# Kernel optimization log

Hardware: AMD Instinct MI355X
Metric: run time of the kernel (lower is better)

## Reference

```python
import jax, jax.numpy as jnp
import numpy as np
import itertools

B, RES, RES_, STRIDE = 256, 14, 7, 2
N, N_ = RES * RES, RES_ * RES_
IN_DIM, OUT_DIM = 384, 512
H, KD, AR = 12, 32, 2
D = AR * KD            # 64, per-head value dim
DH = D * H             # 768
NH_KD = KD * H         # 384
KV_H = DH + NH_KD      # 1152
EPS = 1e-5


def _bias_idxs():
    # Replicates the relative-offset indexing from __init__.
    points = list(itertools.product(range(RES), range(RES)))
    points_ = list(itertools.product(range(RES_), range(RES_)))
    offsets, idxs = {}, []
    for p1 in points_:
        for p2 in points:
            off = (abs(p1[0] * STRIDE - p2[0]), abs(p1[1] * STRIDE - p2[1]))
            if off not in offsets:
                offsets[off] = len(offsets)
            idxs.append(offsets[off])
    return np.array(idxs, dtype=np.int32).reshape(N_, N), len(offsets)


def linear_bn(x, w, gamma, beta, mean, var):
    # Linear (no bias) followed by BatchNorm1d in inference form (fused affine).
    s = gamma / jnp.sqrt(var + EPS)
    return jnp.matmul(x, w.T) * s + (beta - mean * s)


def setup_inputs() -> dict:
    key = jax.random.key(0)
    ks = jax.random.split(key, 12)
    idxs_np, n_off = _bias_idxs()

    def bn_params(k, dim):
        k1, k2, k3, k4 = jax.random.split(k, 4)
        return (jax.random.normal(k1, (dim,)) * 0.1 + 1.0,   # gamma
                jax.random.normal(k2, (dim,)) * 0.1,          # beta
                jax.random.normal(k3, (dim,)) * 0.1,          # running_mean
                jax.random.uniform(k4, (dim,), minval=0.5, maxval=1.5))  # running_var

    kv_g, kv_b, kv_m, kv_v = bn_params(ks[1], KV_H)
    q_g, q_b, q_m, q_v = bn_params(ks[3], NH_KD)
    pr_g, pr_b, pr_m, pr_v = bn_params(ks[5], OUT_DIM)

    return {
        "x": jax.random.normal(ks[0], (B, N, IN_DIM), dtype=jnp.float32),
        "kv_w": jax.random.normal(ks[6], (KV_H, IN_DIM), dtype=jnp.float32) * (IN_DIM ** -0.5),
        "kv_g": kv_g, "kv_b": kv_b, "kv_m": kv_m, "kv_v": kv_v,
        "q_w": jax.random.normal(ks[7], (NH_KD, IN_DIM), dtype=jnp.float32) * (IN_DIM ** -0.5),
        "q_g": q_g, "q_b": q_b, "q_m": q_m, "q_v": q_v,
        "proj_w": jax.random.normal(ks[8], (OUT_DIM, DH), dtype=jnp.float32) * (DH ** -0.5),
        "proj_g": pr_g, "proj_b": pr_b, "proj_m": pr_m, "proj_v": pr_v,
        "attention_biases": jax.random.normal(ks[9], (H, n_off), dtype=jnp.float32) * 0.02,
        "bias_idxs": jnp.asarray(idxs_np),
    }


def reference(x, kv_w, kv_g, kv_b, kv_m, kv_v,
              q_w, q_g, q_b, q_m, q_v,
              proj_w, proj_g, proj_b, proj_m, proj_v,
              attention_biases, bias_idxs):
    Bsz = x.shape[0]
    scale = KD ** -0.5
    # kv projection: [B, N, H, KD+D] -> split into k, v
    kv = linear_bn(x, kv_w, kv_g, kv_b, kv_m, kv_v).reshape(Bsz, N, H, KD + D)
    k, v = kv[..., :KD], kv[..., KD:]
    # strided subsample of queries: [B, 14, 14, C] -> [B, 49, C]
    xs = x.reshape(Bsz, RES, RES, IN_DIM)[:, ::STRIDE, ::STRIDE].reshape(Bsz, N_, IN_DIM)
    q = linear_bn(xs, q_w, q_g, q_b, q_m, q_v).reshape(Bsz, N_, H, KD)
    # attention with gathered relative-position bias: bias [H, N_, N]
    bias = attention_biases[:, bias_idxs]
    attn = jnp.einsum('bqhd,bkhd->bhqk', q, k) * scale + bias
    attn = jax.nn.softmax(attn, axis=-1)
    out = jnp.einsum('bhqk,bkhd->bqhd', attn, v).reshape(Bsz, N_, DH)
    out = jax.nn.hard_swish(out)
    return linear_bn(out, proj_w, proj_g, proj_b, proj_m, proj_v)
```

## Files before the change

kernel.cpp:

```cpp
#include <hip/hip_runtime.h>
#include <hip/hip_bf16.h>
#include <math.h>

typedef unsigned short U16;
typedef unsigned int U32;
typedef __attribute__((ext_vector_type(8))) short bf8;
typedef __attribute__((ext_vector_type(4))) float f4;
typedef __attribute__((ext_vector_type(4))) unsigned short u16x4;

#define AS1 __attribute__((address_space(1)))
#define AS3 __attribute__((address_space(3)))

#define BSZ   256
#define NTOK  196
#define NQ    49
#define INDIM 384
#define OUTD  512
#define NH    12
#define DV    64
#define DHD   768
#define KVH   1152
#define NPADR 224

__device__ inline U16 f2bf(float f){
    __hip_bfloat16 h = __float2bfloat16(f);
    return *(U16*)&h;
}
__device__ inline f4 f4zero(){ f4 z; z[0]=0.f; z[1]=0.f; z[2]=0.f; z[3]=0.f; return z; }
__device__ inline bf8 bf8zero(){ bf8 v;
#pragma unroll
    for (int j=0;j<8;++j) v[j]=0; return v; }

__global__ void k_cast8p(const float* __restrict__ in, U16* __restrict__ out, int n8){
    int i = blockIdx.x*256 + threadIdx.x;
    if (i >= n8) return;
    int rall = i / 48;
    int c8   = i - rall*48;
    int b    = rall / NPADR;
    int r    = rall - b*NPADR;
    U16 o[8];
    if (r < NTOK){
        const float* p = in + ((size_t)(b*NTOK + r))*INDIM + c8*8;
#pragma unroll
        for (int j=0;j<8;++j) o[j] = f2bf(p[j]);
    } else {
#pragma unroll
        for (int j=0;j<8;++j) o[j] = 0;
    }
    *(bf8*)(out + (size_t)i*8) = *(const bf8*)o;
}

#define W1C (KVH*INDIM/8)
#define W2C (INDIM*INDIM/8)
#define W3C (OUTD*DHD/8)
__global__ void k_castw(const float* __restrict__ w1, const float* __restrict__ w2,
                        const float* __restrict__ w3, U16* __restrict__ o1,
                        U16* __restrict__ o2, U16* __restrict__ o3){
    int i = blockIdx.x*256 + threadIdx.x;
    const float* p; U16* o;
    if (i < W1C){ p = w1 + (size_t)i*8; o = o1 + (size_t)i*8; }
    else if (i < W1C+W2C){ int k=i-W1C; p = w2 + (size_t)k*8; o = o2 + (size_t)k*8; }
    else if (i < W1C+W2C+W3C){ int k=i-W1C-W2C; p = w3 + (size_t)k*8; o = o3 + (size_t)k*8; }
    else return;
    U16 t[8];
#pragma unroll
    for (int j=0;j<8;++j) t[j] = f2bf(p[j]);
    *(bf8*)o = *(const bf8*)t;
}

#define BIAS_N   (NH*NQ*NTOK)
#define BIAS_BLK ((BIAS_N+255)/256)
#define BN_BLK   ((KVH+INDIM+OUTD)/256)
__global__ void k_misc(const float* __restrict__ ab, const int* __restrict__ idxs, int n_off,
                       const float* __restrict__ g1, const float* __restrict__ b1,
                       const float* __restrict__ m1, const float* __restrict__ v1,
                       const float* __restrict__ g2, const float* __restrict__ b2,
                       const float* __restrict__ m2, const float* __restrict__ v2,
                       const float* __restrict__ g3, const float* __restrict__ b3,
                       const float* __restrict__ m3, const float* __restrict__ v3,
                       float* __restrict__ s1, float* __restrict__ bo1,
                       float* __restrict__ s2, float* __restrict__ bo2,
                       float* __restrict__ s3, float* __restrict__ bo3,
                       float* __restrict__ bias_out){
    int blk = blockIdx.x;
    int tid = threadIdx.x;
    if (blk < BIAS_BLK){
        int i = blk*256 + tid;
        if (i < BIAS_N){
            int h = i / (NQ*NTOK);
            int qk = i - h*(NQ*NTOK);
            bias_out[i] = ab[h*n_off + idxs[qk]];
        }
    } else {
        int i = (blk-BIAS_BLK)*256 + tid;
        const float *g,*b,*m,*v; float *so,*bo; int k;
        if (i < KVH){ g=g1;b=b1;m=m1;v=v1;so=s1;bo=bo1;k=i; }
        else if (i < KVH+INDIM){ g=g2;b=b2;m=m2;v=v2;so=s2;bo=bo2;k=i-KVH; }
        else { g=g3;b=b3;m=m3;v=v3;so=s3;bo=bo3;k=i-KVH-INDIM; }
        float s = g[k] / sqrtf(v[k] + 1e-5f);
        so[k] = s;
        bo[k] = b[k] - m[k]*s;
    }
}

#define KLO 12800
__global__ __launch_bounds__(256,2) void k_fused(
    const U16* __restrict__ xbf, const U16* __restrict__ kvw, const U16* __restrict__ qo_,
    const float* __restrict__ skv, const float* __restrict__ bkv,
    const float* __restrict__ biasf, U16* __restrict__ aout)
{
    __shared__ U16 smem[20480];
    const int hw = blockIdx.x;
    const int bh = (hw & 7)*384 + (hw >> 3);
    const int b = bh / NH, h = bh - b*NH;
    const int tid = threadIdx.x, lane = tid & 63, w = tid >> 6;
    const int wm = w & 1, wn = w >> 1;
    const int l15 = lane & 15, oct = lane >> 4;

    U16* Ab[2] = { smem + 0,     smem + 7168 };
    U16* Bb[2] = { smem + 14336, smem + 17408 };

    U32 aoff[4];
#pragma unroll
    for (int c=0;c<3;++c){
        int s = c*256 + tid;
        int ach = s / NPADR, ar = s - ach*NPADR;
        aoff[c] = (U32)(b*NPADR + ar)*INDIM + ach*8;
    }
    {
        int s = 768 + (tid & 127);
        int ach = s / NPADR, ar = s - ach*NPADR;
        aoff[3] = (U32)(b*NPADR + ar)*INDIM + ach*8;
    }
    U32 boff[2];
    {
        int s0 = tid;
        int bc0 = s0 / 96, br0 = s0 - bc0*96;
        boff[0] = (U32)(h*96 + br0)*INDIM + bc0*8;
        int s1 = 128 + (tid | 128);
        int bc1 = s1 / 96, br1 = s1 - bc1*96;
        boff[1] = (U32)(h*96 + br1)*INDIM + bc1*8;
    }

    f4 acc[7][3];
#pragma unroll
    for (int i=0;i<7;++i)
#pragma unroll
        for (int j=0;j<3;++j) acc[i][j] = f4zero();

#define STAGE(buf, kb) do{ \
    _Pragma("unroll") \
    for (int c=0;c<3;++c) \
        __builtin_amdgcn_global_load_lds((const AS1 U32*)(xbf + aoff[c] + (kb)), \
            (AS3 U32*)(Ab[buf] + (c*256+tid)*8), 16, 0, 0); \
    if (tid < 128) \
        __builtin_amdgcn_global_load_lds((const AS1 U32*)(xbf + aoff[3] + (kb)), \
            (AS3 U32*)(Ab[buf] + (768+tid)*8), 16, 0, 0); \
    __builtin_amdgcn_global_load_lds((const AS1 U32*)(kvw + boff[0] + (kb)), \
        (AS3 U32*)(Bb[buf] + tid*8), 16, 0, 0); \
    if (tid >= 128) \
        __builtin_amdgcn_global_load_lds((const AS1 U32*)(kvw + boff[1] + (kb)), \
            (AS3 U32*)(Bb[buf] + (128+tid)*8), 16, 0, 0); \
}while(0)

    STAGE(0, 0);

#pragma unroll
    for (int kt=0; kt<12; ++kt){
        const int cur = kt & 1;
        if (kt < 11){
            STAGE(cur^1, (kt+1)*32);
            asm volatile("s_waitcnt vmcnt(5)" ::: "memory");
        } else {
            asm volatile("s_waitcnt vmcnt(0)" ::: "memory");
        }
        __builtin_amdgcn_sched_barrier(0);
        __builtin_amdgcn_s_barrier();
        __builtin_amdgcn_sched_barrier(0);

        bf8 af[7], bfr[3];
#pragma unroll
        for (int i=0;i<7;++i)
            af[i]  = *(const bf8*)(Ab[cur] + (oct*NPADR + wm*112 + i*16 + l15)*8);
#pragma unroll
        for (int j=0;j<3;++j)
            bfr[j] = *(const bf8*)(Bb[cur] + (oct*96 + wn*48 + j*16 + l15)*8);
        __builtin_amdgcn_s_setprio(1);
#pragma unroll
        for (int i=0;i<7;++i)
#pragma unroll
            for (int j=0;j<3;++j)
                acc[i][j] = __builtin_amdgcn_mfma_f32_16x16x32_bf16(af[i], bfr[j], acc[i][j], 0, 0, 0);
        __builtin_amdgcn_s_setprio(0);
        __builtin_amdgcn_sched_barrier(0);
        __builtin_amdgcn_s_barrier();
        __builtin_amdgcn_sched_barrier(0);
    }
#undef STAGE

#pragma unroll
    for (int j=0;j<3;++j){
        const int cc = wn*48 + j*16 + l15;
        const float sc = skv[h*96 + cc];
        const float bi = bkv[h*96 + cc];
#pragma unroll
        for (int i=0;i<7;++i){
            const int n0 = wm*112 + i*16 + oct*4;
            if (cc < 32){
#pragma unroll
                for (int r=0;r<4;++r)
                    smem[KLO + ((cc>>3)*NPADR + n0 + r)*8 + (cc&7)] = f2bf(acc[i][j][r]*sc + bi);
            } else if (n0 < 200){
                const int dv = cc - 32;
                u16x4 pk;
#pragma unroll
                for (int r=0;r<4;++r) pk[r] = f2bf(acc[i][j][r]*sc + bi);
                *(u16x4*)(smem + ((n0>>3)*64 + dv)*8 + (oct&1)*4) = pk;
            }
        }
    }
    __syncthreads();

    const int qg = w*16 + l15;
    bf8 qf = bf8zero();
    if (qg < NQ) qf = *(const bf8*)(qo_ + ((size_t)(b*NQ + qg))*INDIM + h*32 + oct*8);

    f4 sacc[14];
#pragma unroll
    for (int mt=0;mt<14;++mt) sacc[mt] = f4zero();
#pragma unroll
    for (int mt=0;mt<14;++mt){
        const bf8 kf = *(const bf8*)(smem + KLO + (oct*NPADR + mt*16 + l15)*8);
        sacc[mt] = __builtin_amdgcn_mfma_f32_16x16x32_bf16(kf, qf, sacc[mt], 0, 0, 0);
    }

    const float scale = 0.17677669529663689f;
    float mx = -1e30f;
#pragma unroll
    for (int mt=0;mt<14;++mt){
        const int n0 = mt*16 + oct*4;
        f4 bi4 = f4zero();
        if (qg < NQ && n0 < NTOK) bi4 = *(const f4*)(biasf + ((size_t)h*NQ + qg)*NTOK + n0);
#pragma unroll
        for (int r=0;r<4;++r){
            float s = (n0 + r < NTOK) ? sacc[mt][r]*scale + bi4[r] : -1e30f;
            sacc[mt][r] = s;
            mx = fmaxf(mx, s);
        }
    }
    mx = fmaxf(mx, __shfl_xor(mx, 16));
    mx = fmaxf(mx, __shfl_xor(mx, 32));

    float sum = 0.f;
#pragma unroll
    for (int mt=0;mt<14;++mt){
#pragma unroll
        for (int r=0;r<4;++r){
            float p = (mt*16 + oct*4 + r < NTOK) ? __expf(sacc[mt][r] - mx) : 0.f;
            sacc[mt][r] = p;
            sum += p;
        }
    }
    sum += __shfl_xor(sum, 16);
    sum += __shfl_xor(sum, 32);
    const float inv = 1.f / sum;

    const int src1 = l15 + (oct & 1)*32;
    const int src2 = src1 + 16;
    const bool hiT = (oct >> 1) != 0;
    f4 pacc[4];
#pragma unroll
    for (int dt=0;dt<4;++dt) pacc[dt] = f4zero();
#pragma unroll
    for (int kt=0;kt<7;++kt){
        const int m0 = 2*kt, m1 = 2*kt+1;
        U32 q00 = (U32)f2bf(sacc[m0][0]*inv) | ((U32)f2bf(sacc[m0][1]*inv) << 16);
        U32 q01 = (U32)f2bf(sacc[m0][2]*inv) | ((U32)f2bf(sacc[m0][3]*inv) << 16);
        U32 q10 = (U32)f2bf(sacc[m1][0]*inv) | ((U32)f2bf(sacc[m1][1]*inv) << 16);
        U32 q11 = (U32)f2bf(sacc[m1][2]*inv) | ((U32)f2bf(sacc[m1][3]*inv) << 16);
        U32 a0 = __shfl(q00, src1), a1 = __shfl(q01, src1);
        U32 c0 = __shfl(q10, src1), c1 = __shfl(q11, src1);
        U32 b0 = __shfl(q00, src2), b1 = __shfl(q01, src2);
        U32 d0 = __shfl(q10, src2), d1 = __shfl(q11, src2);
        union { U32 u[4]; bf8 v; } pu;
        pu.u[0] = hiT ? c0 : a0;
        pu.u[1] = hiT ? c1 : a1;
        pu.u[2] = hiT ? d0 : b0;
        pu.u[3] = hiT ? d1 : b1;
#pragma unroll
        for (int dt=0;dt<4;++dt){
            const bf8 vf = *(const bf8*)(smem + ((kt*4 + oct)*64 + dt*16 + l15)*8);
            pacc[dt] = __builtin_amdgcn_mfma_f32_16x16x32_bf16(pu.v, vf, pacc[dt], 0, 0, 0);
        }
    }

#pragma unroll
    for (int dt=0;dt<4;++dt){
#pragma unroll
        for (int r=0;r<4;++r){
            const int qo2 = w*16 + oct*4 + r;
            if (qo2 < NQ){
                const int d = dt*16 + l15;
                float v = pacc[dt][r];
                float tt = fminf(fmaxf(v + 3.f, 0.f), 6.f);
                aout[((size_t)(b*NQ + qo2))*DHD + h*DV + d] = f2bf(v * tt * (1.f/6.f));
            }
        }
    }
}

template<int EPI, int NK, int KD, int NTILN, int NWG, bool SUB>
__global__ __launch_bounds__(256,2) void k_g64(
    const U16* __restrict__ A, const U16* __restrict__ Bw,
    const float* __restrict__ s_arr, const float* __restrict__ b_arr,
    U16* __restrict__ o16, float* __restrict__ o32)
{
    __shared__ U16 smem[24576];
    U16* Ab[2] = { smem,          smem + 8192 };
    U16* Bb[2] = { smem + 16384,  smem + 20480 };
    constexpr int QQ = NWG/8, RR = NWG%8;
    const int xcd = blockIdx.x & 7, rest = blockIdx.x >> 3;
    const int l = (xcd < RR ? xcd*(QQ+1) : RR*(QQ+1) + (xcd-RR)*QQ) + rest;
    const int mtl = l / NTILN, ntl = l - mtl*NTILN;
    const int gm0 = mtl*128, gn0 = ntl*64;
    const int tid  = threadIdx.x;
    const int lane = tid & 63;
    const int w    = tid >> 6;
    const int wm   = w & 1, wn = w >> 1;
    const int l15  = lane & 15, oct = lane >> 4;

    f4 acc[4][2];
#pragma unroll
    for (int i=0;i<4;++i)
#pragma unroll
        for (int j=0;j<2;++j) acc[i][j] = f4zero();

    U32 aoff[4], boff[2];
#pragma unroll
    for (int c=0;c<4;++c){
        int slot = c*256 + tid;
        int row = slot & 127, ch = slot >> 7;
        int grow = gm0 + row;
        if (SUB){
            int b2 = grow / NQ, qq = grow - b2*NQ;
            grow = b2*NPADR + 28*(qq/7) + 2*(qq%7);
        }
        aoff[c] = (U32)grow*KD + ch*8;
    }
#pragma unroll
    for (int c=0;c<2;++c){
        int slot = c*256 + tid;
        int row = slot & 63, ch = slot >> 6;
        boff[c] = (U32)(gn0 + row)*KD + ch*8;
    }

#define STG(buf, kb) do{ \
    _Pragma("unroll") \
    for (int c=0;c<4;++c) \
        __builtin_amdgcn_global_load_lds((const AS1 U32*)(A + aoff[c] + (kb)), \
            (AS3 U32*)(Ab[buf] + (c*256+tid)*8), 16, 0, 0); \
    _Pragma("unroll") \
    for (int c=0;c<2;++c) \
        __builtin_amdgcn_global_load_lds((const AS1 U32*)(Bw + boff[c] + (kb)), \
            (AS3 U32*)(Bb[buf] + (c*256+tid)*8), 16, 0, 0); \
}while(0)

    STG(0, 0);

#pragma unroll
    for (int kt=0; kt<NK; ++kt){
        const int cur = kt & 1;
        if (kt+1 < NK){
            STG(cur^1, (kt+1)*64);
            asm volatile("s_waitcnt vmcnt(6)" ::: "memory");
        } else {
            asm volatile("s_waitcnt vmcnt(0)" ::: "memory");
        }
        __builtin_amdgcn_sched_barrier(0);
        __builtin_amdgcn_s_barrier();
        __builtin_amdgcn_sched_barrier(0);

#pragma unroll
        for (int kk=0;kk<2;++kk){
            bf8 af[4], bfr[2];
#pragma unroll
            for (int i=0;i<4;++i)
                af[i]  = *(const bf8*)(Ab[cur] + ((kk*4+oct)*128 + wm*64 + i*16 + l15)*8);
#pragma unroll
            for (int j=0;j<2;++j)
                bfr[j] = *(const bf8*)(Bb[cur] + ((kk*4+oct)*64 + wn*32 + j*16 + l15)*8);
            __builtin_amdgcn_s_setprio(1);
#pragma unroll
            for (int i=0;i<4;++i)
#pragma unroll
                for (int j=0;j<2;++j)
                    acc[i][j] = __builtin_amdgcn_mfma_f32_16x16x32_bf16(af[i], bfr[j], acc[i][j], 0, 0, 0);
            __builtin_amdgcn_s_setprio(0);
        }
        __builtin_amdgcn_sched_barrier(0);
        __builtin_amdgcn_s_barrier();
        __builtin_amdgcn_sched_barrier(0);
    }
#undef STG

#pragma unroll
    for (int j=0;j<2;++j){
        const int col = gn0 + wn*32 + j*16 + l15;
        const float sc = s_arr[col];
        const float bi = b_arr[col];
#pragma unroll
        for (int i=0;i<4;++i){
            const int row0 = gm0 + wm*64 + i*16 + oct*4;
#pragma unroll
            for (int r=0;r<4;++r){
                const float val = acc[i][j][r]*sc + bi;
                if (EPI == 0) o16[(size_t)(row0+r)*INDIM + col] = f2bf(val);
                else          o32[(size_t)(row0+r)*OUTD  + col] = val;
            }
        }
    }
}

extern "C" void kernel_launch(void* const* d_in, const int* in_sizes, int n_in,
                              void* d_out, int out_size, void* d_ws, size_t ws_size,
                              hipStream_t stream)
{
    const float* x    = (const float*)d_in[0];
    const float* kv_w = (const float*)d_in[1];
    const float* kv_g = (const float*)d_in[2];
    const float* kv_b = (const float*)d_in[3];
    const float* kv_m = (const float*)d_in[4];
    const float* kv_v = (const float*)d_in[5];
    const float* q_w  = (const float*)d_in[6];
    const float* q_g  = (const float*)d_in[7];
    const float* q_b  = (const float*)d_in[8];
    const float* q_m  = (const float*)d_in[9];
    const float* q_v  = (const float*)d_in[10];
    const float* pr_w = (const float*)d_in[11];
    const float* pr_g = (const float*)d_in[12];
    const float* pr_b = (const float*)d_in[13];
    const float* pr_m = (const float*)d_in[14];
    const float* pr_v = (const float*)d_in[15];
    const float* ab   = (const float*)d_in[16];
    const int*  idxs  = (const int*)d_in[17];
    const int n_off = in_sizes[16] / NH;

    char* ws = (char*)d_ws;
    size_t off = 0;
    auto alloc = [&](size_t bytes)->char*{
        char* p = ws + off; off += (bytes + 255) & ~(size_t)255; return p;
    };
    U16*   x_bf   = (U16*)  alloc((size_t)BSZ*NPADR*INDIM*2);
    U16*   kvw_bf = (U16*)  alloc((size_t)KVH*INDIM*2);
    U16*   qw_bf  = (U16*)  alloc((size_t)INDIM*INDIM*2);
    U16*   prw_bf = (U16*)  alloc((size_t)OUTD*DHD*2);
    float* s_kv   = (float*)alloc(KVH*4);
    float* b_kv   = (float*)alloc(KVH*4);
    float* s_q    = (float*)alloc(INDIM*4);
    float* b_q    = (float*)alloc(INDIM*4);
    float* s_pr   = (float*)alloc(OUTD*4);
    float* b_pr   = (float*)alloc(OUTD*4);
    float* biasf  = (float*)alloc(((size_t)NH*NQ*NTOK + 256)*4);
    U16*   q_out  = (U16*)  alloc((size_t)BSZ*NQ*INDIM*2);
    U16*   a_out  = (U16*)  alloc((size_t)BSZ*NQ*DHD*2);
    if (off > ws_size) return;

    {
        int n8 = BSZ*NPADR*INDIM/8;
        k_cast8p<<<(n8+255)/256, 256, 0, stream>>>(x, x_bf, n8);
    }
    k_castw<<<(W1C+W2C+W3C+255)/256, 256, 0, stream>>>(kv_w, q_w, pr_w, kvw_bf, qw_bf, prw_bf);
    k_misc<<<BIAS_BLK+BN_BLK, 256, 0, stream>>>(
        ab, idxs, n_off,
        kv_g, kv_b, kv_m, kv_v, q_g, q_b, q_m, q_v, pr_g, pr_b, pr_m, pr_v,
        s_kv, b_kv, s_q, b_q, s_pr, b_pr, biasf);

    k_g64<0, 6, INDIM, 6, 588, true><<<588, 256, 0, stream>>>(
        x_bf, qw_bf, s_q, b_q, q_out, nullptr);
    k_fused<<<BSZ*NH, 256, 0, stream>>>(x_bf, kvw_bf, q_out, s_kv, b_kv, biasf, a_out);
    k_g64<1, 12, DHD, 8, 784, false><<<784, 256, 0, stream>>>(
        a_out, prw_bf, s_pr, b_pr, nullptr, (float*)d_out);
}
```

Before: 192.0 us.

## Fuse fp32-to-bf16 activation cast into Q-projection and fused attention loaders

Drops the standalone kernel that casts and pads x to bf16. The Q-projection GEMM and the fused KV/attention kernel now load fp32 x straight into registers, convert to bf16 and write it to LDS themselves. This removes a full read of x and the write and re-read of a bf16 copy of it. In exchange, every k_fused block reads twice as many A-operand bytes. The pipeline also becomes register-staged with full vmcnt/lgkmcnt waits each iteration, which may weaken the overlap between loads and MFMA work. Padded rows are now clamped to the last token instead of being zero.

```diff
diff --git a/kernel.cpp b/kernel.cpp
--- a/kernel.cpp
+++ b/kernel.cpp
@@ -30,25 +30,6 @@
 __device__ inline bf8 bf8zero(){ bf8 v;
 #pragma unroll
     for (int j=0;j<8;++j) v[j]=0; return v; }
-
-__global__ void k_cast8p(const float* __restrict__ in, U16* __restrict__ out, int n8){
-    int i = blockIdx.x*256 + threadIdx.x;
-    if (i >= n8) return;
-    int rall = i / 48;
-    int c8   = i - rall*48;
-    int b    = rall / NPADR;
-    int r    = rall - b*NPADR;
-    U16 o[8];
-    if (r < NTOK){
-        const float* p = in + ((size_t)(b*NTOK + r))*INDIM + c8*8;
-#pragma unroll
-        for (int j=0;j<8;++j) o[j] = f2bf(p[j]);
-    } else {
-#pragma unroll
-        for (int j=0;j<8;++j) o[j] = 0;
-    }
-    *(bf8*)(out + (size_t)i*8) = *(const bf8*)o;
-}
 
 #define W1C (KVH*INDIM/8)
 #define W2C (INDIM*INDIM/8)
@@ -105,7 +86,7 @@
 
 #define KLO 12800
 __global__ __launch_bounds__(256,2) void k_fused(
-    const U16* __restrict__ xbf, const U16* __restrict__ kvw, const U16* __restrict__ qo_,
+    const float* __restrict__ xf, const U16* __restrict__ kvw, const U16* __restrict__ qo_,
     const float* __restrict__ skv, const float* __restrict__ bkv,
     const float* __restrict__ biasf, U16* __restrict__ aout)
 {
@@ -120,17 +101,19 @@
     U16* Ab[2] = { smem + 0,     smem + 7168 };
     U16* Bb[2] = { smem + 14336, smem + 17408 };
 
-    U32 aoff[4];
+    U32 aoffF[4];
 #pragma unroll
     for (int c=0;c<3;++c){
         int s = c*256 + tid;
         int ach = s / NPADR, ar = s - ach*NPADR;
-        aoff[c] = (U32)(b*NPADR + ar)*INDIM + ach*8;
+        int row = (ar < NTOK) ? ar : (NTOK-1);
+        aoffF[c] = (U32)(b*NTOK + row)*INDIM + ach*8;
     }
     {
         int s = 768 + (tid & 127);
         int ach = s / NPADR, ar = s - ach*NPADR;
-        aoff[3] = (U32)(b*NPADR + ar)*INDIM + ach*8;
+        int row = (ar < NTOK) ? ar : (NTOK-1);
+        aoffF[3] = (U32)(b*NTOK + row)*INDIM + ach*8;
     }
     U32 boff[2];
     {
@@ -142,20 +125,42 @@
         boff[1] = (U32)(h*96 + br1)*INDIM + bc1*8;
     }
 
+    f4 areg[4][2];
     f4 acc[7][3];
 #pragma unroll
     for (int i=0;i<7;++i)
 #pragma unroll
         for (int j=0;j<3;++j) acc[i][j] = f4zero();
 
-#define STAGE(buf, kb) do{ \
+#define LOAD_A(kb) do{ \
     _Pragma("unroll") \
-    for (int c=0;c<3;++c) \
-        __builtin_amdgcn_global_load_lds((const AS1 U32*)(xbf + aoff[c] + (kb)), \
-            (AS3 U32*)(Ab[buf] + (c*256+tid)*8), 16, 0, 0); \
-    if (tid < 128) \
-        __builtin_amdgcn_global_load_lds((const AS1 U32*)(xbf + aoff[3] + (kb)), \
-            (AS3 U32*)(Ab[buf] + (768+tid)*8), 16, 0, 0); \
+    for (int c=0;c<3;++c){ \
+        const float* p = xf + aoffF[c] + (kb); \
+        areg[c][0] = *(const f4*)p; areg[c][1] = *(const f4*)(p+4); \
+    } \
+    if (tid < 128){ \
+        const float* p = xf + aoffF[3] + (kb); \
+        areg[3][0] = *(const f4*)p; areg[3][1] = *(const f4*)(p+4); \
+    } \
+}while(0)
+
+#define WRITE_A(buf) do{ \
+    _Pragma("unroll") \
+    for (int c=0;c<3;++c){ \
+        U16 t[8]; \
+        _Pragma("unroll") \
+        for (int j=0;j<4;++j){ t[j] = f2bf(areg[c][0][j]); t[4+j] = f2bf(areg[c][1][j]); } \
+        *(bf8*)(Ab[buf] + (c*256+tid)*8) = *(const bf8*)t; \
+    } \
+    if (tid < 128){ \
+        U16 t[8]; \
+        _Pragma("unroll") \
+        for (int j=0;j<4;++j){ t[j] = f2bf(areg[3][0][j]); t[4+j] = f2bf(areg[3][1][j]); } \
+        *(bf8*)(Ab[buf] + (768+tid)*8) = *(const bf8*)t; \
+    } \
+}while(0)
+
+#define ISSUE_B(buf, kb) do{ \
     __builtin_amdgcn_global_load_lds((const AS1 U32*)(kvw + boff[0] + (kb)), \
         (AS3 U32*)(Bb[buf] + tid*8), 16, 0, 0); \
     if (tid >= 128) \
@@ -163,21 +168,23 @@
             (AS3 U32*)(Bb[buf] + (128+tid)*8), 16, 0, 0); \
 }while(0)
 
-    STAGE(0, 0);
+    LOAD_A(0);
+    ISSUE_B(0, 0);
+    WRITE_A(0);
+    asm volatile("s_waitcnt vmcnt(0)" ::: "memory");
+    asm volatile("s_waitcnt lgkmcnt(0)" ::: "memory");
+    __builtin_amdgcn_sched_barrier(0);
+    __builtin_amdgcn_s_barrier();
+    __builtin_amdgcn_sched_barrier(0);
 
 #pragma unroll
     for (int kt=0; kt<12; ++kt){
         const int cur = kt & 1;
         if (kt < 11){
-            STAGE(cur^1, (kt+1)*32);
-            asm volatile("s_waitcnt vmcnt(5)" ::: "memory");
-        } else {
-            asm volatile("s_waitcnt vmcnt(0)" ::: "memory");
-        }
-        __builtin_amdgcn_sched_barrier(0);
-        __builtin_amdgcn_s_barrier();
-        __builtin_amdgcn_sched_barrier(0);
-
+            LOAD_A((kt+1)*32);
+            ISSUE_B(cur^1, (kt+1)*32);
+        }
+        __builtin_amdgcn_sched_barrier(0);
         bf8 af[7], bfr[3];
 #pragma unroll
         for (int i=0;i<7;++i)
@@ -193,10 +200,16 @@
                 acc[i][j] = __builtin_amdgcn_mfma_f32_16x16x32_bf16(af[i], bfr[j], acc[i][j], 0, 0, 0);
         __builtin_amdgcn_s_setprio(0);
         __builtin_amdgcn_sched_barrier(0);
+        if (kt < 11) WRITE_A(cur^1);
+        asm volatile("s_waitcnt vmcnt(0)" ::: "memory");
+        asm volatile("s_waitcnt lgkmcnt(0)" ::: "memory");
+        __builtin_amdgcn_sched_barrier(0);
         __builtin_amdgcn_s_barrier();
         __builtin_amdgcn_sched_barrier(0);
     }
-#undef STAGE
+#undef LOAD_A
+#undef WRITE_A
+#undef ISSUE_B
 
 #pragma unroll
     for (int j=0;j<3;++j){
@@ -309,19 +322,18 @@
     }
 }
 
-template<int EPI, int NK, int KD, int NTILN, int NWG, bool SUB>
-__global__ __launch_bounds__(256,2) void k_g64(
-    const U16* __restrict__ A, const U16* __restrict__ Bw,
+__global__ __launch_bounds__(256,2) void k_qg(
+    const float* __restrict__ xf, const U16* __restrict__ Bw,
     const float* __restrict__ s_arr, const float* __restrict__ b_arr,
-    U16* __restrict__ o16, float* __restrict__ o32)
+    U16* __restrict__ o16)
 {
     __shared__ U16 smem[24576];
     U16* Ab[2] = { smem,          smem + 8192 };
     U16* Bb[2] = { smem + 16384,  smem + 20480 };
-    constexpr int QQ = NWG/8, RR = NWG%8;
+    constexpr int NWG = 588, QQ = NWG/8, RR = NWG%8;
     const int xcd = blockIdx.x & 7, rest = blockIdx.x >> 3;
     const int l = (xcd < RR ? xcd*(QQ+1) : RR*(QQ+1) + (xcd-RR)*QQ) + rest;
-    const int mtl = l / NTILN, ntl = l - mtl*NTILN;
+    const int mtl = l / 6, ntl = l - mtl*6;
     const int gm0 = mtl*128, gn0 = ntl*64;
     const int tid  = threadIdx.x;
     const int lane = tid & 63;
@@ -329,29 +341,153 @@
     const int wm   = w & 1, wn = w >> 1;
     const int l15  = lane & 15, oct = lane >> 4;
 
+    f4 areg[4][2];
     f4 acc[4][2];
 #pragma unroll
     for (int i=0;i<4;++i)
 #pragma unroll
         for (int j=0;j<2;++j) acc[i][j] = f4zero();
 
-    U32 aoff[4], boff[2];
+    U32 aoffF[4], boff[2];
 #pragma unroll
     for (int c=0;c<4;++c){
         int slot = c*256 + tid;
         int row = slot & 127, ch = slot >> 7;
         int grow = gm0 + row;
-        if (SUB){
-            int b2 = grow / NQ, qq = grow - b2*NQ;
-            grow = b2*NPADR + 28*(qq/7) + 2*(qq%7);
-        }
-        aoff[c] = (U32)grow*KD + ch*8;
+        int b2 = grow / NQ, qq = grow - b2*NQ;
+        int xrow = b2*NTOK + 28*(qq/7) + 2*(qq%7);
+        aoffF[c] = (U32)xrow*INDIM + ch*8;
     }
 #pragma unroll
     for (int c=0;c<2;++c){
         int slot = c*256 + tid;
         int row = slot & 63, ch = slot >> 6;
-        boff[c] = (U32)(gn0 + row)*KD + ch*8;
+        boff[c] = (U32)(gn0 + row)*INDIM + ch*8;
+    }
+
+#define QLOAD_A(kb) do{ \
+    _Pragma("unroll") \
+    for (int c=0;c<4;++c){ \
+        const float* p = xf + aoffF[c] + (kb); \
+        areg[c][0] = *(const f4*)p; areg[c][1] = *(const f4*)(p+4); \
+    } \
+}while(0)
+
+#define QWRITE_A(buf) do{ \
+    _Pragma("unroll") \
+    for (int c=0;c<4;++c){ \
+        U16 t[8]; \
+        _Pragma("unroll") \
+        for (int j=0;j<4;++j){ t[j] = f2bf(areg[c][0][j]); t[4+j] = f2bf(areg[c][1][j]); } \
+        *(bf8*)(Ab[buf] + (c*256+tid)*8) = *(const bf8*)t; \
+    } \
+}while(0)
+
+#define QISSUE_B(buf, kb) do{ \
+    _Pragma("unroll") \
+    for (int c=0;c<2;++c) \
+        __builtin_amdgcn_global_load_lds((const AS1 U32*)(Bw + boff[c] + (kb)), \
+            (AS3 U32*)(Bb[buf] + (c*256+tid)*8), 16, 0, 0); \
+}while(0)
+
+    QLOAD_A(0);
+    QISSUE_B(0, 0);
+    QWRITE_A(0);
+    asm volatile("s_waitcnt vmcnt(0)" ::: "memory");
+    asm volatile("s_waitcnt lgkmcnt(0)" ::: "memory");
+    __builtin_amdgcn_sched_barrier(0);
+    __builtin_amdgcn_s_barrier();
+    __builtin_amdgcn_sched_barrier(0);
+
+#pragma unroll
+    for (int kt=0; kt<6; ++kt){
+        const int cur = kt & 1;
+        if (kt < 5){
+            QLOAD_A((kt+1)*64);
+            QISSUE_B(cur^1, (kt+1)*64);
+        }
+        __builtin_amdgcn_sched_barrier(0);
+#pragma unroll
+        for (int kk=0;kk<2;++kk){
+            bf8 af[4], bfr[2];
+#pragma unroll
+            for (int i=0;i<4;++i)
+                af[i]  = *(const bf8*)(Ab[cur] + ((kk*4+oct)*128 + wm*64 + i*16 + l15)*8);
+#pragma unroll
+            for (int j=0;j<2;++j)
+                bfr[j] = *(const bf8*)(Bb[cur] + ((kk*4+oct)*64 + wn*32 + j*16 + l15)*8);
+            __builtin_amdgcn_s_setprio(1);
+#pragma unroll
+            for (int i=0;i<4;++i)
+#pragma unroll
+                for (int j=0;j<2;++j)
+                    acc[i][j] = __builtin_amdgcn_mfma_f32_16x16x32_bf16(af[i], bfr[j], acc[i][j], 0, 0, 0);
+            __builtin_amdgcn_s_setprio(0);
+        }
+        __builtin_amdgcn_sched_barrier(0);
+        if (kt < 5) QWRITE_A(cur^1);
+        asm volatile("s_waitcnt vmcnt(0)" ::: "memory");
+        asm volatile("s_waitcnt lgkmcnt(0)" ::: "memory");
+        __builtin_amdgcn_sched_barrier(0);
+        __builtin_amdgcn_s_barrier();
+        __builtin_amdgcn_sched_barrier(0);
+    }
+#undef QLOAD_A
+#undef QWRITE_A
+#undef QISSUE_B
+
+#pragma unroll
+    for (int j=0;j<2;++j){
+        const int col = gn0 + wn*32 + j*16 + l15;
+        const float sc = s_arr[col];
+        const float bi = b_arr[col];
+#pragma unroll
+        for (int i=0;i<4;++i){
+            const int row0 = gm0 + wm*64 + i*16 + oct*4;
+#pragma unroll
+            for (int r=0;r<4;++r)
+                o16[(size_t)(row0+r)*INDIM + col] = f2bf(acc[i][j][r]*sc + bi);
+        }
+    }
+}
+
+__global__ __launch_bounds__(256,2) void k_proj(
+    const U16* __restrict__ A, const U16* __restrict__ Bw,
+    const float* __restrict__ s_arr, const float* __restrict__ b_arr,
+    float* __restrict__ o32)
+{
+    __shared__ U16 smem[24576];
+    U16* Ab[2] = { smem,          smem + 8192 };
+    U16* Bb[2] = { smem + 16384,  smem + 20480 };
+    constexpr int NWG = 784, QQ = NWG/8, RR = NWG%8;
+    const int xcd = blockIdx.x & 7, rest = blockIdx.x >> 3;
+    const int l = (xcd < RR ? xcd*(QQ+1) : RR*(QQ+1) + (xcd-RR)*QQ) + rest;
+    const int mtl = l / 8, ntl = l - mtl*8;
+    const int gm0 = mtl*128, gn0 = ntl*64;
+    const int tid  = threadIdx.x;
+    const int lane = tid & 63;
+    const int w    = tid >> 6;
+    const int wm   = w & 1, wn = w >> 1;
+    const int l15  = lane & 15, oct = lane >> 4;
+
+    f4 acc[4][2];
+#pragma unroll
+    for (int i=0;i<4;++i)
+#pragma unroll
+        for (int j=0;j<2;++j) acc[i][j] = f4zero();
+
+    U32 aoff[4], boff[2];
+#pragma unroll
+    for (int c=0;c<4;++c){
+        int slot = c*256 + tid;
+        int row = slot & 127, ch = slot >> 7;
+        aoff[c] = (U32)(gm0 + row)*DHD + ch*8;
+    }
+#pragma unroll
+    for (int c=0;c<2;++c){
+        int slot = c*256 + tid;
+        int row = slot & 63, ch = slot >> 6;
+        boff[c] = (U32)(gn0 + row)*DHD + ch*8;
     }
 
 #define STG(buf, kb) do{ \
@@ -368,9 +504,9 @@
     STG(0, 0);
 
 #pragma unroll
-    for (int kt=0; kt<NK; ++kt){
+    for (int kt=0; kt<12; ++kt){
         const int cur = kt & 1;
-        if (kt+1 < NK){
+        if (kt+1 < 12){
             STG(cur^1, (kt+1)*64);
             asm volatile("s_waitcnt vmcnt(6)" ::: "memory");
         } else {
@@ -412,11 +548,8 @@
         for (int i=0;i<4;++i){
             const int row0 = gm0 + wm*64 + i*16 + oct*4;
 #pragma unroll
-            for (int r=0;r<4;++r){
-                const float val = acc[i][j][r]*sc + bi;
-                if (EPI == 0) o16[(size_t)(row0+r)*INDIM + col] = f2bf(val);
-                else          o32[(size_t)(row0+r)*OUTD  + col] = val;
-            }
+            for (int r=0;r<4;++r)
+                o32[(size_t)(row0+r)*OUTD + col] = acc[i][j][r]*sc + bi;
         }
     }
 }
@@ -450,7 +583,6 @@
     auto alloc = [&](size_t bytes)->char*{
         char* p = ws + off; off += (bytes + 255) & ~(size_t)255; return p;
     };
-    U16*   x_bf   = (U16*)  alloc((size_t)BSZ*NPADR*INDIM*2);
     U16*   kvw_bf = (U16*)  alloc((size_t)KVH*INDIM*2);
     U16*   qw_bf  = (U16*)  alloc((size_t)INDIM*INDIM*2);
     U16*   prw_bf = (U16*)  alloc((size_t)OUTD*DHD*2);
@@ -465,19 +597,13 @@
     U16*   a_out  = (U16*)  alloc((size_t)BSZ*NQ*DHD*2);
     if (off > ws_size) return;
 
-    {
-        int n8 = BSZ*NPADR*INDIM/8;
-        k_cast8p<<<(n8+255)/256, 256, 0, stream>>>(x, x_bf, n8);
-    }
     k_castw<<<(W1C+W2C+W3C+255)/256, 256, 0, stream>>>(kv_w, q_w, pr_w, kvw_bf, qw_bf, prw_bf);
     k_misc<<<BIAS_BLK+BN_BLK, 256, 0, stream>>>(
         ab, idxs, n_off,
         kv_g, kv_b, kv_m, kv_v, q_g, q_b, q_m, q_v, pr_g, pr_b, pr_m, pr_v,
         s_kv, b_kv, s_q, b_q, s_pr, b_pr, biasf);
 
-    k_g64<0, 6, INDIM, 6, 588, true><<<588, 256, 0, stream>>>(
-        x_bf, qw_bf, s_q, b_q, q_out, nullptr);
-    k_fused<<<BSZ*NH, 256, 0, stream>>>(x_bf, kvw_bf, q_out, s_kv, b_kv, biasf, a_out);
-    k_g64<1, 12, DHD, 8, 784, false><<<784, 256, 0, stream>>>(
-        a_out, prw_bf, s_pr, b_pr, nullptr, (float*)d_out);
+    k_qg<<<588, 256, 0, stream>>>(x, qw_bf, s_q, b_q, q_out);
+    k_fused<<<BSZ*NH, 256, 0, stream>>>(x, kvw_bf, q_out, s_kv, b_kv, biasf, a_out);
+    k_proj<<<784, 256, 0, stream>>>(a_out, prw_bf, s_pr, b_pr, (float*)d_out);
 }
```

After: 244.7 us. 27.5% more time.
